# Optimization experiments

Measured on AMD Instinct MI355X. Metric: run time of the kernel, lower is better.

Reference implementation:

```python
import jax, jax.numpy as jnp
import numpy as np

HEADS = 16
DIM_HEAD = 64
EXPANSION = 2
WINDOW = 512


def setup_inputs() -> dict:
    key = jax.random.key(0)
    ks = jax.random.split(key, 9)
    b, n, dim_q, dim_kv = 2, 2048, 1024, 1024
    di = HEADS * DIM_HEAD          # 1024
    dm = di * EXPANSION            # 2048
    def w(k, shape, fan_in):
        return jax.random.normal(k, shape, jnp.float32) * (fan_in ** -0.5)
    return {
        "queries_input": jax.random.normal(ks[0], (b, n, dim_q), jnp.float32),
        "key_values_input": jax.random.normal(ks[1], (b, n, dim_kv), jnp.float32),
        "Wq": w(ks[2], (dim_q, di), dim_q),
        "Wk1": w(ks[3], (dim_kv, di), dim_kv),
        "Wv1": w(ks[4], (dim_kv, dm), dim_kv),
        "Wk2": w(ks[5], (dim_kv, dm), dim_kv),
        "Wv2": w(ks[6], (dim_kv, di), dim_kv),
        "Wout": w(ks[7], (di, dim_q), di),
        "attn_sink": jax.random.normal(ks[8], (HEADS,), jnp.float32) * 0.01,
    }


def _split_heads(t):
    # b n (h d) -> b h n d
    b, n, _ = t.shape
    return t.reshape(b, n, HEADS, -1).transpose(0, 2, 1, 3)


def _attend(q, k, v, attn_sink, window):
    scale = DIM_HEAD ** -0.5  # fixed at dim_head**-0.5 in both attends, as in the original
    sim = jnp.einsum('bhid,bhjd->bhij', q * scale, k)
    b, _, n, _ = sim.shape
    idx = jnp.arange(n)
    # faithful to original mask indexing (i==j case): mask where j>i and j-i<=window
    mask = (idx[None, :] > idx[:, None]) & (idx[None, :] - idx[:, None] <= window)
    sim = jnp.where(mask, -jnp.finfo(sim.dtype).max, sim)
    # prepend learned per-head sink logit, softmax, then drop the sink column
    sink_col = jnp.broadcast_to(attn_sink[None, :, None, None], (b, HEADS, n, 1))
    attn = jax.nn.softmax(jnp.concatenate([sink_col, sim], axis=-1), axis=-1)[..., 1:]
    return jnp.einsum('bhij,bhjd->bhid', attn, v)


def reference(queries_input, key_values_input, Wq, Wk1, Wv1, Wk2, Wv2, Wout, attn_sink):
    q = _split_heads(queries_input @ Wq)        # [b,h,n,64]
    k1 = _split_heads(key_values_input @ Wk1)   # [b,h,n,64]
    v1 = _split_heads(key_values_input @ Wv1)   # [b,h,n,128]
    k2 = _split_heads(key_values_input @ Wk2)   # [b,h,n,128]
    v2 = _split_heads(key_values_input @ Wv2)   # [b,h,n,64]
    hiddens = _attend(q, k1, v1, attn_sink, WINDOW)     # [b,h,n,128]
    hiddens = jax.nn.silu(hiddens)                       # implicit MLP activation
    out = _attend(hiddens, k2, v2, attn_sink, WINDOW)    # [b,h,n,64]
    b, _, n, _ = out.shape
    out = out.transpose(0, 2, 1, 3).reshape(b, n, -1)    # merge heads
    return out @ Wout
```

## Files before the change

### kernel.cpp

```cpp
#include <hip/hip_runtime.h>
#include <cstddef>
#include <cstdint>

#define NSEQ 2048
#define NB 2
#define NH 16
#define WINDOW 512

#define LOG2E 1.44269504088896f
#define QSCALE 0.180336877396f

typedef __attribute__((ext_vector_type(8))) short short8;
typedef __attribute__((ext_vector_type(4))) float f32x4;
typedef __attribute__((ext_vector_type(4))) unsigned short ushort4v;

__device__ __forceinline__ unsigned short f2bf(float f) {
    union { float f; unsigned u; } v; v.f = f;
    unsigned r = v.u + 0x7FFFu + ((v.u >> 16) & 1u);
    return (unsigned short)(r >> 16);
}

__device__ __forceinline__ unsigned cvt_pk_bf16(float a, float b) {
    unsigned r;
    asm("v_cvt_pk_bf16_f32 %0, %1, %2" : "=v"(r) : "v"(a), "v"(b));
    return r;
}

typedef const __attribute__((address_space(1))) unsigned int* gasp;
typedef __attribute__((address_space(3))) unsigned int* lasp;
__device__ __forceinline__ void gll16(const void* g, void* l) {
    __builtin_amdgcn_global_load_lds((gasp)g, (lasp)l, 16, 0, 0);
}

__device__ __forceinline__ f32x4 mfma16(short8 a, short8 b, f32x4 c) {
    return __builtin_amdgcn_mfma_f32_16x16x32_bf16(a, b, c, 0, 0, 0);
}

__global__ __launch_bounds__(256)
void castk(const float* __restrict__ in, unsigned short* __restrict__ out, int n4) {
    int i = blockIdx.x * 256 + threadIdx.x;
    if (i < n4) {
        float4 v = ((const float4*)in)[i];
        ushort4v o;
        o[0] = f2bf(v.x); o[1] = f2bf(v.y); o[2] = f2bf(v.z); o[3] = f2bf(v.w);
        ((ushort4v*)out)[i] = o;
    }
}

__global__ __launch_bounds__(256)
void wtrans(const float* __restrict__ Wsrc, unsigned short* __restrict__ Wt, int K, int N) {
    __shared__ float tile[32][33];
    const int tx = threadIdx.x, ty = threadIdx.y;
    const int n0 = blockIdx.x * 32, k0 = blockIdx.y * 32;
#pragma unroll
    for (int i = 0; i < 4; ++i)
        tile[ty + i * 8][tx] = Wsrc[(size_t)(k0 + ty + i * 8) * N + n0 + tx];
    __syncthreads();
#pragma unroll
    for (int i = 0; i < 4; ++i)
        Wt[(size_t)(n0 + ty + i * 8) * K + k0 + tx] = f2bf(tile[tx][ty + i * 8]);
}

#define OUT_F32 0
#define OUT_BF16 1
#define OUT_KV 2

template <int OMODE>
__global__ __launch_bounds__(256)
void gemm_bf16(const unsigned short* __restrict__ A,
               const unsigned short* __restrict__ Bt,
               void* __restrict__ Cout, int K, int ldc, float oscale,
               unsigned short* __restrict__ K1p, unsigned short* __restrict__ V1t,
               unsigned short* __restrict__ K2p, unsigned short* __restrict__ V2t)
{
    __shared__ __align__(16) unsigned short As[128 * 32];
    __shared__ __align__(16) unsigned short Bs[128 * 32];
    const int t = threadIdx.x;
    const int l = t & 63, w = t >> 6;
    const int q = l & 15, g = l >> 4;
    const int bm = blockIdx.y * 128, bn = blockIdx.x * 128;
    const int wm = (w & 1) * 64, wn = (w >> 1) * 64;

    f32x4 acc[4][4];
    const f32x4 zero = {0.f, 0.f, 0.f, 0.f};
#pragma unroll
    for (int i = 0; i < 4; ++i)
#pragma unroll
        for (int j = 0; j < 4; ++j) acc[i][j] = zero;

    const unsigned short* Abase = A + (size_t)bm * K;
    const unsigned short* Bbase = Bt + (size_t)bn * K;

    for (int k0 = 0; k0 < K; k0 += 32) {
        __syncthreads();
#pragma unroll
        for (int it = 0; it < 2; ++it) {
            int c = w * 128 + it * 64 + l;
            int r = c >> 2, sg = c & 3;
            gll16(Abase + (size_t)r * K + k0 + sg * 8, (char*)As + c * 16);
            gll16(Bbase + (size_t)r * K + k0 + sg * 8, (char*)Bs + c * 16);
        }
        __syncthreads();
        short8 a[4], b[4];
#pragma unroll
        for (int ms = 0; ms < 4; ++ms)
            a[ms] = *(const short8*)(As + (wm + ms * 16 + q) * 32 + g * 8);
#pragma unroll
        for (int ns = 0; ns < 4; ++ns)
            b[ns] = *(const short8*)(Bs + (wn + ns * 16 + q) * 32 + g * 8);
#pragma unroll
        for (int ms = 0; ms < 4; ++ms)
#pragma unroll
            for (int ns = 0; ns < 4; ++ns)
                acc[ms][ns] = mfma16(a[ms], b[ns], acc[ms][ns]);
    }

    if constexpr (OMODE == OUT_F32) {
        float* C = (float*)Cout;
#pragma unroll
        for (int ms = 0; ms < 4; ++ms)
#pragma unroll
            for (int r = 0; r < 4; ++r) {
                int row = bm + wm + ms * 16 + g * 4 + r;
                float* crow = C + (size_t)row * ldc + bn + wn;
#pragma unroll
                for (int ns = 0; ns < 4; ++ns) crow[ns * 16 + q] = acc[ms][ns][r] * oscale;
            }
    } else if constexpr (OMODE == OUT_BF16) {
        unsigned short* C = (unsigned short*)Cout;
#pragma unroll
        for (int ms = 0; ms < 4; ++ms)
#pragma unroll
            for (int r = 0; r < 4; ++r) {
                int row = bm + wm + ms * 16 + g * 4 + r;
                unsigned short* crow = C + (size_t)row * ldc + bn + wn;
#pragma unroll
                for (int ns = 0; ns < 4; ++ns) crow[ns * 16 + q] = f2bf(acc[ms][ns][r] * oscale);
            }
    } else {
        const int colbase = bn + wn;
        if (colbase < 1024) {
#pragma unroll
            for (int ms = 0; ms < 4; ++ms)
#pragma unroll
                for (int r = 0; r < 4; ++r) {
                    int row = bm + wm + ms * 16 + g * 4 + r;
                    unsigned short* crow = K1p + (size_t)row * 1024 + colbase;
#pragma unroll
                    for (int ns = 0; ns < 4; ++ns) crow[ns * 16 + q] = f2bf(acc[ms][ns][r]);
                }
        } else if (colbase < 3072) {
#pragma unroll
            for (int ms = 0; ms < 4; ++ms) {
                int row0 = bm + wm + ms * 16 + g * 4;
                int bb = row0 >> 11, nn = row0 & 2047;
#pragma unroll
                for (int ns = 0; ns < 4; ++ns) {
                    int c2 = colbase - 1024 + ns * 16 + q;
                    int h = c2 >> 7, d = c2 & 127;
                    ushort4v pk;
#pragma unroll
                    for (int r = 0; r < 4; ++r) pk[r] = f2bf(acc[ms][ns][r]);
                    *(ushort4v*)(V1t + ((size_t)((bb * NH + h) * 128 + d)) * NSEQ + nn) = pk;
                }
            }
        } else if (colbase < 5120) {
#pragma unroll
            for (int ms = 0; ms < 4; ++ms)
#pragma unroll
                for (int r = 0; r < 4; ++r) {
                    int row = bm + wm + ms * 16 + g * 4 + r;
                    unsigned short* crow = K2p + (size_t)row * 2048 + colbase - 3072;
#pragma unroll
                    for (int ns = 0; ns < 4; ++ns) crow[ns * 16 + q] = f2bf(acc[ms][ns][r]);
                }
        } else {
#pragma unroll
            for (int ms = 0; ms < 4; ++ms) {
                int row0 = bm + wm + ms * 16 + g * 4;
                int bb = row0 >> 11, nn = row0 & 2047;
#pragma unroll
                for (int ns = 0; ns < 4; ++ns) {
                    int c2 = colbase - 5120 + ns * 16 + q;
                    int h = c2 >> 6, d = c2 & 63;
                    ushort4v pk;
#pragma unroll
                    for (int r = 0; r < 4; ++r) pk[r] = f2bf(acc[ms][ns][r]);
                    *(ushort4v*)(V2t + ((size_t)((bb * NH + h) * 64 + d)) * NSEQ + nn) = pk;
                }
            }
        }
    }
}

template <int DK, int DV, bool SILU, bool Q_PH, bool O_PH>
__global__ __launch_bounds__(256)
void attend_mfma(const unsigned short* __restrict__ Qg,
                 const unsigned short* __restrict__ Kg,
                 const unsigned short* __restrict__ Vtg,
                 const float* __restrict__ sink,
                 unsigned short* __restrict__ Og)
{
    constexpr int KT = 64;
    constexpr int NS = DV / 16;
    constexpr int NDB = DK / 32;
    constexpr int KROWB = DK * 2;
    constexpr int KSEGS = KROWB / 16;

    __shared__ __align__(16) char KsB[64 * DK * 2];
    __shared__ __align__(16) char VtB[DV * 64 * 2];
    __shared__ __align__(16) char PsB[64 * 128];

    const int t = threadIdx.x, l = t & 63, w = t >> 6;
    const int q = l & 15, g = l >> 4;
    const int bh = blockIdx.x, bi = bh >> 4, h = bh & 15;
    const int i0 = blockIdx.y * 64;
    const int iq = i0 + w * 16 + q;
    const int qrow = w * 16 + q;

    const unsigned short* qbase;
    if constexpr (Q_PH)
        qbase = Qg + ((size_t)((bi * NH + h) * NSEQ + iq)) * DK;
    else
        qbase = Qg + ((size_t)(bi * NSEQ + iq)) * (NH * DK) + h * DK;
    short8 qf[NDB];
#pragma unroll
    for (int db = 0; db < NDB; ++db)
        qf[db] = *(const short8*)(qbase + db * 32 + g * 8);

    float m = sink[h] * LOG2E, lsum = 1.0f;
    f32x4 o[NS];
    const f32x4 zero = {0.f, 0.f, 0.f, 0.f};
#pragma unroll
    for (int ns = 0; ns < NS; ++ns) o[ns] = zero;

    const unsigned short* kbase = Kg + (size_t)(bi * NSEQ) * (NH * DK) + h * DK;
    const unsigned short* vbase = Vtg + (size_t)((bi * NH + h) * DV) * NSEQ;

    for (int j0 = 0; j0 < NSEQ; j0 += KT) {
        const int dd = j0 - i0;
        if (dd >= KT && dd <= WINDOW - KT) continue;

        __syncthreads();
#pragma unroll
        for (int it = 0; it < (64 * KSEGS) / 256; ++it) {
            int c = w * (64 * KSEGS / 4) + it * 64 + l;
            int kv = c / KSEGS, sgst = c % KSEGS;
            int sgsrc = sgst ^ (kv & 7);
            gll16(kbase + (size_t)(j0 + kv) * (NH * DK) + sgsrc * 8, KsB + c * 16);
        }
#pragma unroll
        for (int it = 0; it < (DV * 8) / 256; ++it) {
            int c = w * (DV * 8 / 4) + it * 64 + l;
            int d = c >> 3, sgst = c & 7;
            int sgsrc = sgst ^ (d & 7);
            gll16(vbase + (size_t)d * NSEQ + j0 + sgsrc * 8, VtB + c * 16);
        }
        __syncthreads();

        float st[4][4];
#pragma unroll
        for (int s = 0; s < 4; ++s) {
            f32x4 sacc = zero;
            int kvr = s * 16 + q;
#pragma unroll
            for (int db = 0; db < NDB; ++db) {
                short8 kf = *(const short8*)(KsB + kvr * KROWB + (((db * 4 + g) ^ (kvr & 7)) << 4));
                sacc = mfma16(kf, qf[db], sacc);
            }
#pragma unroll
            for (int r = 0; r < 4; ++r) st[s][r] = sacc[r];
        }

        if (dd == 0 || dd == WINDOW) {
#pragma unroll
            for (int s = 0; s < 4; ++s)
#pragma unroll
                for (int r = 0; r < 4; ++r) {
                    int j = j0 + s * 16 + g * 4 + r;
                    if (j > iq && (j - iq) <= WINDOW) st[s][r] = -3.0e38f;
                }
        }

        float mx = st[0][0];
#pragma unroll
        for (int s = 0; s < 4; ++s)
#pragma unroll
            for (int r = 0; r < 4; ++r)
                if (s || r) mx = fmaxf(mx, st[s][r]);
        mx = fmaxf(mx, __shfl_xor(mx, 16));
        mx = fmaxf(mx, __shfl_xor(mx, 32));

        if (!__all(mx - m <= 8.0f)) {
            const float nm = fmaxf(m, mx);
            const float corr = exp2f(m - nm);
            m = nm;
            lsum *= corr;
            float cr[4];
#pragma unroll
            for (int r = 0; r < 4; ++r) cr[r] = __shfl(corr, g * 4 + r);
#pragma unroll
            for (int ns = 0; ns < NS; ++ns)
#pragma unroll
                for (int r = 0; r < 4; ++r) o[ns][r] *= cr[r];
        }

        float ps = 0.f;
#pragma unroll
        for (int s = 0; s < 4; ++s) {
            float p0 = exp2f(st[s][0] - m);
            float p1 = exp2f(st[s][1] - m);
            float p2 = exp2f(st[s][2] - m);
            float p3 = exp2f(st[s][3] - m);
            ps += (p0 + p1) + (p2 + p3);
            uint2 pk;
            pk.x = cvt_pk_bf16(p0, p1);
            pk.y = cvt_pk_bf16(p2, p3);
            *(uint2*)(PsB + qrow * 128 + ((s * 32 + g * 8) ^ ((q & 7) << 4))) = pk;
        }
        ps += __shfl_xor(ps, 16);
        ps += __shfl_xor(ps, 32);
        lsum += ps;

#pragma unroll
        for (int kb = 0; kb < 2; ++kb) {
            short8 pf = *(const short8*)(PsB + qrow * 128 + ((((kb * 4 + g) ^ (q & 7))) << 4));
#pragma unroll
            for (int ns = 0; ns < NS; ++ns) {
                int d = ns * 16 + q;
                short8 vf = *(const short8*)(VtB + d * 128 + (((kb * 4 + g) ^ (d & 7)) << 4));
                o[ns] = mfma16(pf, vf, o[ns]);
            }
        }
    }

    const float inv = 1.0f / lsum;
    float ivr[4];
#pragma unroll
    for (int r = 0; r < 4; ++r) ivr[r] = __shfl(inv, g * 4 + r);
#pragma unroll
    for (int ns = 0; ns < NS; ++ns)
#pragma unroll
        for (int r = 0; r < 4; ++r) {
            float x = o[ns][r] * ivr[r];
            if constexpr (SILU) x = x / (1.0f + __expf(-x)) * QSCALE;
            int qr = i0 + w * 16 + g * 4 + r;
            int d = ns * 16 + q;
            size_t off;
            if constexpr (O_PH)
                off = ((size_t)((bi * NH + h) * NSEQ + qr)) * DV + d;
            else
                off = ((size_t)(bi * NSEQ + qr)) * (NH * DV) + h * DV + d;
            Og[off] = f2bf(x);
        }
}

extern "C" void kernel_launch(void* const* d_in, const int* in_sizes, int n_in,
                              void* d_out, int out_size, void* d_ws, size_t ws_size,
                              hipStream_t stream)
{
    (void)in_sizes; (void)n_in; (void)out_size; (void)ws_size;
    const float* queries = (const float*)d_in[0];
    const float* kvin    = (const float*)d_in[1];
    const float* Wq      = (const float*)d_in[2];
    const float* Wk1     = (const float*)d_in[3];
    const float* Wv1     = (const float*)d_in[4];
    const float* Wk2     = (const float*)d_in[5];
    const float* Wv2     = (const float*)d_in[6];
    const float* Wout    = (const float*)d_in[7];
    const float* sink    = (const float*)d_in[8];
    float* out = (float*)d_out;

    unsigned short* Xq   = (unsigned short*)d_ws;
    unsigned short* Xkv  = Xq   + (size_t)4096 * 1024;
    unsigned short* Wqt  = Xkv  + (size_t)4096 * 1024;
    unsigned short* Wk1t = Wqt  + (size_t)1024 * 1024;
    unsigned short* Wv1t = Wk1t + (size_t)1024 * 1024;
    unsigned short* Wk2t = Wv1t + (size_t)2048 * 1024;
    unsigned short* Wv2t = Wk2t + (size_t)2048 * 1024;
    unsigned short* Wot  = Wv2t + (size_t)1024 * 1024;
    unsigned short* Qp   = Wot  + (size_t)1024 * 1024;
    unsigned short* K1p  = Qp   + (size_t)4096 * 1024;
    unsigned short* V1t  = K1p  + (size_t)4096 * 1024;
    unsigned short* K2p  = V1t  + (size_t)2 * 16 * 128 * 2048;
    unsigned short* V2t  = K2p  + (size_t)4096 * 2048;
    unsigned short* Hb   = V2t  + (size_t)2 * 16 * 64 * 2048;
    unsigned short* AO   = Hb   + (size_t)2 * 16 * 2048 * 128;

    dim3 blk(256);
    dim3 tblk(32, 8);

    castk<<<4096, blk, 0, stream>>>(queries, Xq, 1048576);
    castk<<<4096, blk, 0, stream>>>(kvin, Xkv, 1048576);
    wtrans<<<dim3(32, 32), tblk, 0, stream>>>(Wq,   Wqt,  1024, 1024);
    wtrans<<<dim3(32, 32), tblk, 0, stream>>>(Wk1,  Wk1t, 1024, 1024);
    wtrans<<<dim3(64, 32), tblk, 0, stream>>>(Wv1,  Wv1t, 1024, 2048);
    wtrans<<<dim3(64, 32), tblk, 0, stream>>>(Wk2,  Wk2t, 1024, 2048);
    wtrans<<<dim3(32, 32), tblk, 0, stream>>>(Wv2,  Wv2t, 1024, 1024);
    wtrans<<<dim3(32, 32), tblk, 0, stream>>>(Wout, Wot,  1024, 1024);

    gemm_bf16<OUT_BF16><<<dim3(8, 32), blk, 0, stream>>>(
        Xq, Wqt, Qp, 1024, 1024, QSCALE, nullptr, nullptr, nullptr, nullptr);
    gemm_bf16<OUT_KV><<<dim3(48, 32), blk, 0, stream>>>(
        Xkv, Wk1t, nullptr, 1024, 0, 1.0f, K1p, V1t, K2p, V2t);

    attend_mfma<64, 128, true, false, true><<<dim3(32, 32), blk, 0, stream>>>(
        Qp, K1p, V1t, sink, Hb);
    attend_mfma<128, 64, false, true, false><<<dim3(32, 32), blk, 0, stream>>>(
        Hb, K2p, V2t, sink, AO);

    gemm_bf16<OUT_F32><<<dim3(8, 32), blk, 0, stream>>>(
        AO, Wot, out, 1024, 1024, 1.0f, nullptr, nullptr, nullptr, nullptr);
}
```

Before: 426.2 us.

## Merge prep kernels, fuse Q into projection GEMM, double-buffer K tiles in attention

The two input casts become one launch, and the six weight transposes become another. The Q projection is folded into the combined KV projection GEMM, which works because the transposed weights sit next to each other in the workspace. In attention, the loop now visits only the unmasked key tiles instead of skipping masked ones inside it. K tiles are double-buffered through global-to-LDS loads, and V fragments are read straight from global memory into registers instead of being staged in LDS. This cuts launch overhead and hides K load latency, at the cost of higher register pressure and uncoalesced direct V reads.

```diff
diff --git a/kernel.cpp b/kernel.cpp
--- a/kernel.cpp
+++ b/kernel.cpp
@@ -37,42 +37,55 @@
 }
 
 __global__ __launch_bounds__(256)
-void castk(const float* __restrict__ in, unsigned short* __restrict__ out, int n4) {
+void castk2(const float* __restrict__ a, const float* __restrict__ b,
+            unsigned short* __restrict__ oa, unsigned short* __restrict__ ob) {
     int i = blockIdx.x * 256 + threadIdx.x;
-    if (i < n4) {
-        float4 v = ((const float4*)in)[i];
-        ushort4v o;
-        o[0] = f2bf(v.x); o[1] = f2bf(v.y); o[2] = f2bf(v.z); o[3] = f2bf(v.w);
-        ((ushort4v*)out)[i] = o;
-    }
+    const float* src = a; unsigned short* dst = oa;
+    if (i >= 1048576) { src = b; dst = ob; i -= 1048576; }
+    float4 v = ((const float4*)src)[i];
+    ushort4v o;
+    o[0] = f2bf(v.x); o[1] = f2bf(v.y); o[2] = f2bf(v.z); o[3] = f2bf(v.w);
+    ((ushort4v*)dst)[i] = o;
 }
 
 __global__ __launch_bounds__(256)
-void wtrans(const float* __restrict__ Wsrc, unsigned short* __restrict__ Wt, int K, int N) {
+void wtrans_all(const float* __restrict__ Wq, const float* __restrict__ Wk1,
+                const float* __restrict__ Wv1, const float* __restrict__ Wk2,
+                const float* __restrict__ Wv2, const float* __restrict__ Wout,
+                unsigned short* __restrict__ Wqt, unsigned short* __restrict__ Wk1t,
+                unsigned short* __restrict__ Wv1t, unsigned short* __restrict__ Wk2t,
+                unsigned short* __restrict__ Wv2t, unsigned short* __restrict__ Wot)
+{
     __shared__ float tile[32][33];
-    const int tx = threadIdx.x, ty = threadIdx.y;
-    const int n0 = blockIdx.x * 32, k0 = blockIdx.y * 32;
+    int id = blockIdx.x;
+    const float* S; unsigned short* D; int N;
+    if (id < 1024)      { S = Wq;   D = Wqt;  N = 1024; }
+    else if (id < 2048) { S = Wk1;  D = Wk1t; N = 1024; id -= 1024; }
+    else if (id < 4096) { S = Wv1;  D = Wv1t; N = 2048; id -= 2048; }
+    else if (id < 6144) { S = Wk2;  D = Wk2t; N = 2048; id -= 4096; }
+    else if (id < 7168) { S = Wv2;  D = Wv2t; N = 1024; id -= 6144; }
+    else                { S = Wout; D = Wot;  N = 1024; id -= 7168; }
+    const int nt = N >> 5;
+    const int n0 = (id & (nt - 1)) << 5;
+    const int k0 = (id / nt) << 5;
+    const int tx = threadIdx.x & 31, ty = threadIdx.x >> 5;
 #pragma unroll
     for (int i = 0; i < 4; ++i)
-        tile[ty + i * 8][tx] = Wsrc[(size_t)(k0 + ty + i * 8) * N + n0 + tx];
+        tile[ty + i * 8][tx] = S[(size_t)(k0 + ty + i * 8) * N + n0 + tx];
     __syncthreads();
 #pragma unroll
     for (int i = 0; i < 4; ++i)
-        Wt[(size_t)(n0 + ty + i * 8) * K + k0 + tx] = f2bf(tile[tx][ty + i * 8]);
-}
-
-#define OUT_F32 0
-#define OUT_BF16 1
-#define OUT_KV 2
-
-template <int OMODE>
+        D[(size_t)(n0 + ty + i * 8) * 1024 + k0 + tx] = f2bf(tile[tx][ty + i * 8]);
+}
+
 __global__ __launch_bounds__(256)
-void gemm_bf16(const unsigned short* __restrict__ A,
+void gemm_proj(const unsigned short* __restrict__ Aq, const unsigned short* __restrict__ Akv,
                const unsigned short* __restrict__ Bt,
-               void* __restrict__ Cout, int K, int ldc, float oscale,
+               unsigned short* __restrict__ Qp,
                unsigned short* __restrict__ K1p, unsigned short* __restrict__ V1t,
                unsigned short* __restrict__ K2p, unsigned short* __restrict__ V2t)
 {
+    constexpr int K = 1024;
     __shared__ __align__(16) unsigned short As[128 * 32];
     __shared__ __align__(16) unsigned short Bs[128 * 32];
     const int t = threadIdx.x;
@@ -88,7 +101,7 @@
 #pragma unroll
         for (int j = 0; j < 4; ++j) acc[i][j] = zero;
 
-    const unsigned short* Abase = A + (size_t)bm * K;
+    const unsigned short* Abase = ((bn < 1024) ? Aq : Akv) + (size_t)bm * K;
     const unsigned short* Bbase = Bt + (size_t)bn * K;
 
     for (int k0 = 0; k0 < K; k0 += 32) {
@@ -115,82 +128,126 @@
                 acc[ms][ns] = mfma16(a[ms], b[ns], acc[ms][ns]);
     }
 
-    if constexpr (OMODE == OUT_F32) {
-        float* C = (float*)Cout;
+    const int colbase = bn + wn;
+    if (colbase < 1024) {
 #pragma unroll
         for (int ms = 0; ms < 4; ++ms)
 #pragma unroll
             for (int r = 0; r < 4; ++r) {
                 int row = bm + wm + ms * 16 + g * 4 + r;
-                float* crow = C + (size_t)row * ldc + bn + wn;
-#pragma unroll
-                for (int ns = 0; ns < 4; ++ns) crow[ns * 16 + q] = acc[ms][ns][r] * oscale;
-            }
-    } else if constexpr (OMODE == OUT_BF16) {
-        unsigned short* C = (unsigned short*)Cout;
+                unsigned short* crow = Qp + (size_t)row * 1024 + colbase;
+#pragma unroll
+                for (int ns = 0; ns < 4; ++ns) crow[ns * 16 + q] = f2bf(acc[ms][ns][r] * QSCALE);
+            }
+    } else if (colbase < 2048) {
 #pragma unroll
         for (int ms = 0; ms < 4; ++ms)
 #pragma unroll
             for (int r = 0; r < 4; ++r) {
                 int row = bm + wm + ms * 16 + g * 4 + r;
-                unsigned short* crow = C + (size_t)row * ldc + bn + wn;
-#pragma unroll
-                for (int ns = 0; ns < 4; ++ns) crow[ns * 16 + q] = f2bf(acc[ms][ns][r] * oscale);
+                unsigned short* crow = K1p + (size_t)row * 1024 + colbase - 1024;
+#pragma unroll
+                for (int ns = 0; ns < 4; ++ns) crow[ns * 16 + q] = f2bf(acc[ms][ns][r]);
+            }
+    } else if (colbase < 4096) {
+#pragma unroll
+        for (int ms = 0; ms < 4; ++ms) {
+            int row0 = bm + wm + ms * 16 + g * 4;
+            int bb = row0 >> 11, nn = row0 & 2047;
+#pragma unroll
+            for (int ns = 0; ns < 4; ++ns) {
+                int c2 = colbase - 2048 + ns * 16 + q;
+                int h = c2 >> 7, d = c2 & 127;
+                ushort4v pk;
+#pragma unroll
+                for (int r = 0; r < 4; ++r) pk[r] = f2bf(acc[ms][ns][r]);
+                *(ushort4v*)(V1t + ((size_t)((bb * NH + h) * 128 + d)) * NSEQ + nn) = pk;
+            }
+        }
+    } else if (colbase < 6144) {
+#pragma unroll
+        for (int ms = 0; ms < 4; ++ms)
+#pragma unroll
+            for (int r = 0; r < 4; ++r) {
+                int row = bm + wm + ms * 16 + g * 4 + r;
+                unsigned short* crow = K2p + (size_t)row * 2048 + colbase - 4096;
+#pragma unroll
+                for (int ns = 0; ns < 4; ++ns) crow[ns * 16 + q] = f2bf(acc[ms][ns][r]);
             }
     } else {
-        const int colbase = bn + wn;
-        if (colbase < 1024) {
-#pragma unroll
-            for (int ms = 0; ms < 4; ++ms)
-#pragma unroll
-                for (int r = 0; r < 4; ++r) {
-                    int row = bm + wm + ms * 16 + g * 4 + r;
-                    unsigned short* crow = K1p + (size_t)row * 1024 + colbase;
-#pragma unroll
-                    for (int ns = 0; ns < 4; ++ns) crow[ns * 16 + q] = f2bf(acc[ms][ns][r]);
-                }
-        } else if (colbase < 3072) {
-#pragma unroll
-            for (int ms = 0; ms < 4; ++ms) {
-                int row0 = bm + wm + ms * 16 + g * 4;
-                int bb = row0 >> 11, nn = row0 & 2047;
-#pragma unroll
-                for (int ns = 0; ns < 4; ++ns) {
-                    int c2 = colbase - 1024 + ns * 16 + q;
-                    int h = c2 >> 7, d = c2 & 127;
-                    ushort4v pk;
-#pragma unroll
-                    for (int r = 0; r < 4; ++r) pk[r] = f2bf(acc[ms][ns][r]);
-                    *(ushort4v*)(V1t + ((size_t)((bb * NH + h) * 128 + d)) * NSEQ + nn) = pk;
-                }
-            }
-        } else if (colbase < 5120) {
-#pragma unroll
-            for (int ms = 0; ms < 4; ++ms)
-#pragma unroll
-                for (int r = 0; r < 4; ++r) {
-                    int row = bm + wm + ms * 16 + g * 4 + r;
-                    unsigned short* crow = K2p + (size_t)row * 2048 + colbase - 3072;
-#pragma unroll
-                    for (int ns = 0; ns < 4; ++ns) crow[ns * 16 + q] = f2bf(acc[ms][ns][r]);
-                }
-        } else {
-#pragma unroll
-            for (int ms = 0; ms < 4; ++ms) {
-                int row0 = bm + wm + ms * 16 + g * 4;
-                int bb = row0 >> 11, nn = row0 & 2047;
-#pragma unroll
-                for (int ns = 0; ns < 4; ++ns) {
-                    int c2 = colbase - 5120 + ns * 16 + q;
-                    int h = c2 >> 6, d = c2 & 63;
-                    ushort4v pk;
-#pragma unroll
-                    for (int r = 0; r < 4; ++r) pk[r] = f2bf(acc[ms][ns][r]);
-                    *(ushort4v*)(V2t + ((size_t)((bb * NH + h) * 64 + d)) * NSEQ + nn) = pk;
-                }
+#pragma unroll
+        for (int ms = 0; ms < 4; ++ms) {
+            int row0 = bm + wm + ms * 16 + g * 4;
+            int bb = row0 >> 11, nn = row0 & 2047;
+#pragma unroll
+            for (int ns = 0; ns < 4; ++ns) {
+                int c2 = colbase - 6144 + ns * 16 + q;
+                int h = c2 >> 6, d = c2 & 63;
+                ushort4v pk;
+#pragma unroll
+                for (int r = 0; r < 4; ++r) pk[r] = f2bf(acc[ms][ns][r]);
+                *(ushort4v*)(V2t + ((size_t)((bb * NH + h) * 64 + d)) * NSEQ + nn) = pk;
             }
         }
     }
+}
+
+__global__ __launch_bounds__(256)
+void gemm_out(const unsigned short* __restrict__ A, const unsigned short* __restrict__ Bt,
+              float* __restrict__ C)
+{
+    constexpr int K = 1024;
+    __shared__ __align__(16) unsigned short As[128 * 32];
+    __shared__ __align__(16) unsigned short Bs[128 * 32];
+    const int t = threadIdx.x;
+    const int l = t & 63, w = t >> 6;
+    const int q = l & 15, g = l >> 4;
+    const int bm = blockIdx.y * 128, bn = blockIdx.x * 128;
+    const int wm = (w & 1) * 64, wn = (w >> 1) * 64;
+
+    f32x4 acc[4][4];
+    const f32x4 zero = {0.f, 0.f, 0.f, 0.f};
+#pragma unroll
+    for (int i = 0; i < 4; ++i)
+#pragma unroll
+        for (int j = 0; j < 4; ++j) acc[i][j] = zero;
+
+    const unsigned short* Abase = A + (size_t)bm * K;
+    const unsigned short* Bbase = Bt + (size_t)bn * K;
+
+    for (int k0 = 0; k0 < K; k0 += 32) {
+        __syncthreads();
+#pragma unroll
+        for (int it = 0; it < 2; ++it) {
+            int c = w * 128 + it * 64 + l;
+            int r = c >> 2, sg = c & 3;
+            gll16(Abase + (size_t)r * K + k0 + sg * 8, (char*)As + c * 16);
+            gll16(Bbase + (size_t)r * K + k0 + sg * 8, (char*)Bs + c * 16);
+        }
+        __syncthreads();
+        short8 a[4], b[4];
+#pragma unroll
+        for (int ms = 0; ms < 4; ++ms)
+            a[ms] = *(const short8*)(As + (wm + ms * 16 + q) * 32 + g * 8);
+#pragma unroll
+        for (int ns = 0; ns < 4; ++ns)
+            b[ns] = *(const short8*)(Bs + (wn + ns * 16 + q) * 32 + g * 8);
+#pragma unroll
+        for (int ms = 0; ms < 4; ++ms)
+#pragma unroll
+            for (int ns = 0; ns < 4; ++ns)
+                acc[ms][ns] = mfma16(a[ms], b[ns], acc[ms][ns]);
+    }
+
+#pragma unroll
+    for (int ms = 0; ms < 4; ++ms)
+#pragma unroll
+        for (int r = 0; r < 4; ++r) {
+            int row = bm + wm + ms * 16 + g * 4 + r;
+            float* crow = C + (size_t)row * 1024 + bn + wn;
+#pragma unroll
+            for (int ns = 0; ns < 4; ++ns) crow[ns * 16 + q] = acc[ms][ns][r];
+        }
 }
 
 template <int DK, int DV, bool SILU, bool Q_PH, bool O_PH>
@@ -201,14 +258,15 @@
                  const float* __restrict__ sink,
                  unsigned short* __restrict__ Og)
 {
-    constexpr int KT = 64;
     constexpr int NS = DV / 16;
     constexpr int NDB = DK / 32;
     constexpr int KROWB = DK * 2;
     constexpr int KSEGS = KROWB / 16;
-
-    __shared__ __align__(16) char KsB[64 * DK * 2];
-    __shared__ __align__(16) char VtB[DV * 64 * 2];
+    constexpr int KBUF = 64 * KROWB;
+    constexpr int NCH = (64 * KSEGS) / 256;
+    constexpr int KSTRIDE = NH * DK;
+
+    __shared__ __align__(16) char KsB[2 * KBUF];
     __shared__ __align__(16) char PsB[64 * 128];
 
     const int t = threadIdx.x, l = t & 63, w = t >> 6;
@@ -228,51 +286,79 @@
     for (int db = 0; db < NDB; ++db)
         qf[db] = *(const short8*)(qbase + db * 32 + g * 8);
 
+    const unsigned short* kbase = Kg + (size_t)(bi * NSEQ) * KSTRIDE + h * DK;
+    const unsigned short* ksrc[NCH];
+    int kdst[NCH];
+#pragma unroll
+    for (int it = 0; it < NCH; ++it) {
+        int c = w * (NCH * 64) + it * 64 + l;
+        int kv = c / KSEGS, sg = (c % KSEGS) ^ (kv & 7);
+        ksrc[it] = kbase + kv * KSTRIDE + sg * 8;
+        kdst[it] = c * 16;
+    }
+    int kro[NDB];
+#pragma unroll
+    for (int db = 0; db < NDB; ++db)
+        kro[db] = q * KROWB + (((db * 4 + g) ^ (q & 7)) << 4);
+    int pw[4], pr[2];
+#pragma unroll
+    for (int s = 0; s < 4; ++s) pw[s] = qrow * 128 + ((s * 32 + g * 8) ^ ((q & 7) << 4));
+#pragma unroll
+    for (int kb = 0; kb < 2; ++kb) pr[kb] = qrow * 128 + (((kb * 4 + g) ^ (q & 7)) << 4);
+    const unsigned short* vbase = Vtg + (size_t)((bi * NH + h) * DV) * NSEQ;
+    const unsigned short* vp[NS];
+#pragma unroll
+    for (int ns = 0; ns < NS; ++ns) vp[ns] = vbase + (ns * 16 + q) * NSEQ + g * 8;
+
     float m = sink[h] * LOG2E, lsum = 1.0f;
     f32x4 o[NS];
     const f32x4 zero = {0.f, 0.f, 0.f, 0.f};
 #pragma unroll
     for (int ns = 0; ns < NS; ++ns) o[ns] = zero;
 
-    const unsigned short* kbase = Kg + (size_t)(bi * NSEQ) * (NH * DK) + h * DK;
-    const unsigned short* vbase = Vtg + (size_t)((bi * NH + h) * DV) * NSEQ;
-
-    for (int j0 = 0; j0 < NSEQ; j0 += KT) {
-        const int dd = j0 - i0;
-        if (dd >= KT && dd <= WINDOW - KT) continue;
-
+    const int nA = (i0 >> 6) + 1;
+    const int jB = i0 + WINDOW;
+    const int nB = (jB < NSEQ) ? ((NSEQ - jB) >> 6) : 0;
+    const int ntot = nA + nB;
+
+    auto J0 = [&](int tt) { return (tt < nA) ? (tt << 6) : (jB + ((tt - nA) << 6)); };
+    auto stageK = [&](int j0n, int bb) {
+#pragma unroll
+        for (int it = 0; it < NCH; ++it)
+            gll16(ksrc[it] + (size_t)j0n * KSTRIDE, KsB + bb * KBUF + kdst[it]);
+    };
+
+    stageK(0, 0);
+    int buf = 0;
+
+    for (int tt = 0; tt < ntot; ++tt) {
+        const int j0 = J0(tt);
         __syncthreads();
-#pragma unroll
-        for (int it = 0; it < (64 * KSEGS) / 256; ++it) {
-            int c = w * (64 * KSEGS / 4) + it * 64 + l;
-            int kv = c / KSEGS, sgst = c % KSEGS;
-            int sgsrc = sgst ^ (kv & 7);
-            gll16(kbase + (size_t)(j0 + kv) * (NH * DK) + sgsrc * 8, KsB + c * 16);
-        }
-#pragma unroll
-        for (int it = 0; it < (DV * 8) / 256; ++it) {
-            int c = w * (DV * 8 / 4) + it * 64 + l;
-            int d = c >> 3, sgst = c & 7;
-            int sgsrc = sgst ^ (d & 7);
-            gll16(vbase + (size_t)d * NSEQ + j0 + sgsrc * 8, VtB + c * 16);
-        }
-        __syncthreads();
-
+
+        short8 vf[NS][2];
+#pragma unroll
+        for (int ns = 0; ns < NS; ++ns) {
+            const unsigned short* vpt = vp[ns] + j0;
+            vf[ns][0] = *(const short8*)vpt;
+            vf[ns][1] = *(const short8*)(vpt + 32);
+        }
+        if (tt + 1 < ntot) stageK(J0(tt + 1), buf ^ 1);
+
+        const int bo = buf * KBUF;
         float st[4][4];
 #pragma unroll
         for (int s = 0; s < 4; ++s) {
             f32x4 sacc = zero;
-            int kvr = s * 16 + q;
 #pragma unroll
             for (int db = 0; db < NDB; ++db) {
-                short8 kf = *(const short8*)(KsB + kvr * KROWB + (((db * 4 + g) ^ (kvr & 7)) << 4));
+                short8 kf = *(const short8*)(KsB + bo + s * (16 * KROWB) + kro[db]);
                 sacc = mfma16(kf, qf[db], sacc);
             }
 #pragma unroll
             for (int r = 0; r < 4; ++r) st[s][r] = sacc[r];
         }
 
-        if (dd == 0 || dd == WINDOW) {
+        if (j0 == i0 || j0 == jB) {
 #pragma unroll
             for (int s = 0; s < 4; ++s)
 #pragma unroll
@@ -316,7 +402,7 @@
             uint2 pk;
             pk.x = cvt_pk_bf16(p0, p1);
             pk.y = cvt_pk_bf16(p2, p3);
-            *(uint2*)(PsB + qrow * 128 + ((s * 32 + g * 8) ^ ((q & 7) << 4))) = pk;
+            *(uint2*)(PsB + pw[s]) = pk;
         }
         ps += __shfl_xor(ps, 16);
         ps += __shfl_xor(ps, 32);
@@ -324,14 +410,12 @@
 
 #pragma unroll
         for (int kb = 0; kb < 2; ++kb) {
-            short8 pf = *(const short8*)(PsB + qrow * 128 + ((((kb * 4 + g) ^ (q & 7))) << 4));
-#pragma unroll
-            for (int ns = 0; ns < NS; ++ns) {
-                int d = ns * 16 + q;
-                short8 vf = *(const short8*)(VtB + d * 128 + (((kb * 4 + g) ^ (d & 7)) << 4));
-                o[ns] = mfma16(pf, vf, o[ns]);
-            }
-        }
+            short8 pf = *(const short8*)(PsB + pr[kb]);
+#pragma unroll
+            for (int ns = 0; ns < NS; ++ns)
+                o[ns] = mfma16(pf, vf[ns][kb], o[ns]);
+        }
+        buf ^= 1;
     }
 
     const float inv = 1.0f / lsum;
@@ -388,27 +472,17 @@
     unsigned short* AO   = Hb   + (size_t)2 * 16 * 2048 * 128;
 
     dim3 blk(256);
-    dim3 tblk(32, 8);
-
-    castk<<<4096, blk, 0, stream>>>(queries, Xq, 1048576);
-    castk<<<4096, blk, 0, stream>>>(kvin, Xkv, 1048576);
-    wtrans<<<dim3(32, 32), tblk, 0, stream>>>(Wq,   Wqt,  1024, 1024);
-    wtrans<<<dim3(32, 32), tblk, 0, stream>>>(Wk1,  Wk1t, 1024, 1024);
-    wtrans<<<dim3(64, 32), tblk, 0, stream>>>(Wv1,  Wv1t, 1024, 2048);
-    wtrans<<<dim3(64, 32), tblk, 0, stream>>>(Wk2,  Wk2t, 1024, 2048);
-    wtrans<<<dim3(32, 32), tblk, 0, stream>>>(Wv2,  Wv2t, 1024, 1024);
-    wtrans<<<dim3(32, 32), tblk, 0, stream>>>(Wout, Wot,  1024, 1024);
-
-    gemm_bf16<OUT_BF16><<<dim3(8, 32), blk, 0, stream>>>(
-        Xq, Wqt, Qp, 1024, 1024, QSCALE, nullptr, nullptr, nullptr, nullptr);
-    gemm_bf16<OUT_KV><<<dim3(48, 32), blk, 0, stream>>>(
-        Xkv, Wk1t, nullptr, 1024, 0, 1.0f, K1p, V1t, K2p, V2t);
+
+    castk2<<<8192, blk, 0, stream>>>(queries, kvin, Xq, Xkv);
+    wtrans_all<<<8192, blk, 0, stream>>>(Wq, Wk1, Wv1, Wk2, Wv2, Wout,
+                                         Wqt, Wk1t, Wv1t, Wk2t, Wv2t, Wot);
+
+    gemm_proj<<<dim3(56, 32), blk, 0, stream>>>(Xq, Xkv, Wqt, Qp, K1p, V1t, K2p, V2t);
 
     attend_mfma<64, 128, true, false, true><<<dim3(32, 32), blk, 0, stream>>>(
         Qp, K1p, V1t, sink, Hb);
     attend_mfma<128, 64, false, true, false><<<dim3(32, 32), blk, 0, stream>>>(
         Hb, K2p, V2t, sink, AO);
 
-    gemm_bf16<OUT_F32><<<dim3(8, 32), blk, 0, stream>>>(
-        AO, Wot, out, 1024, 1024, 1.0f, nullptr, nullptr, nullptr, nullptr);
-}
+    gemm_out<<<dim3(8, 32), blk, 0, stream>>>(AO, Wot, out);
+}
```

Result: slower. 584.6 us (+37.2%).
